# Performance work log

Measured on AMD Instinct MI355X. Metric: run time of the kernel, lower is better.

## Reference

```python
import jax, jax.numpy as jnp
import numpy as np


def _gcn_conv(X, src, dst, norm, W, n_nodes):
    # gather + normalized aggregate (SpMM) then dense linear (GEMM)
    msg = X[src] * norm[:, None]                       # [E, F]
    agg = jax.ops.segment_sum(msg, dst, num_segments=n_nodes)  # [N, F]
    return agg @ W                                     # [N, F_out]


def setup_inputs() -> dict:
    key = jax.random.key(0)
    k1, k2, k3, k4, k5 = jax.random.split(key, 5)
    N, E, D_IN, D_HID, D_OUT = 50000, 800000, 128, 128, 64
    X = jax.random.normal(k1, (N, D_IN), dtype=jnp.float32)
    edge_index = jax.random.randint(k2, (2, E), 0, N, dtype=jnp.int64)
    s = 1.0 / np.sqrt(D_IN)
    W1 = jax.random.normal(k3, (D_IN, D_HID), dtype=jnp.float32) * s
    W2 = jax.random.normal(k4, (D_HID, D_HID), dtype=jnp.float32) * s
    W3 = jax.random.normal(k5, (D_HID, D_OUT), dtype=jnp.float32) * s
    return {"X": X, "edge_index": edge_index, "W1": W1, "W2": W2, "W3": W3}


def reference(X, edge_index, W1, W2, W3):
    n_nodes = X.shape[0]
    src, dst = edge_index[0], edge_index[1]
    # symmetric degree normalization D^-1/2 A D^-1/2 (degrees from edge list)
    ones = jnp.ones(src.shape[0], dtype=X.dtype)
    deg = jax.ops.segment_sum(ones, dst, num_segments=n_nodes)
    deg = jnp.maximum(deg, 1.0)
    dinv = jax.lax.rsqrt(deg)
    norm = dinv[src] * dinv[dst]                       # [E]
    h = jax.nn.relu(_gcn_conv(X, src, dst, norm, W1, n_nodes))
    h = jax.nn.relu(_gcn_conv(h, src, dst, norm, W2, n_nodes))
    h = jax.nn.relu(_gcn_conv(h, src, dst, norm, W3, n_nodes))
    return jax.nn.softmax(h, axis=-1)
```

## Files before the change

kernel.cpp:

```cpp
#include <hip/hip_runtime.h>
#include <hip/hip_bf16.h>

typedef __attribute__((ext_vector_type(8))) short short8;
typedef __attribute__((ext_vector_type(4))) float f32x4;

static inline size_t ws_align(size_t x) { return (x + 511) & ~((size_t)511); }

static __device__ inline unsigned short f2bf(float f) {
    __hip_bfloat16 h = __float2bfloat16(f);
    return __builtin_bit_cast(unsigned short, h);
}

static __device__ inline float bf2f(unsigned short u) {
    unsigned int x = ((unsigned int)u) << 16;
    return __builtin_bit_cast(float, x);
}

__global__ void sniff_kernel(const unsigned short* __restrict__ w1,
                             const unsigned int* __restrict__ ei,
                             int* __restrict__ flags) {
    int i = threadIdx.x;
    unsigned e = (w1[2 * i] >> 7) & 0xFF;
    unsigned long long m1 = __ballot(e >= 100 && e <= 130);
    unsigned long long m2 = __ballot(ei[2 * i + 1] == 0u);
    if (i == 0) {
        flags[0] = (__popcll(m1) < 48) ? 1 : 0;
        flags[1] = (__popcll(m2) >= 48) ? 1 : 0;
    }
}

__global__ __launch_bounds__(256) void wconv_kernel(const void* __restrict__ W1raw,
                                                    const void* __restrict__ W2raw,
                                                    const void* __restrict__ W3raw,
                                                    const int* __restrict__ flags,
                                                    unsigned short* __restrict__ wt1,
                                                    unsigned short* __restrict__ wt2,
                                                    unsigned short* __restrict__ wt3) {
    int idx = blockIdx.x * 256 + threadIdx.x;
    int in_fp32 = flags[0];
    const void* src;
    unsigned short* dst;
    int e, fout;
    if (idx < 16384) {
        src = W1raw; dst = wt1; e = idx; fout = 128;
    } else if (idx < 32768) {
        src = W2raw; dst = wt2; e = idx - 16384; fout = 128;
    } else if (idx < 40960) {
        src = W3raw; dst = wt3; e = idx - 32768; fout = 64;
    } else {
        return;
    }
    int n = e & (fout - 1);
    int k = e / fout;
    unsigned short v;
    if (in_fp32) v = f2bf(((const float*)src)[e]);
    else         v = ((const unsigned short*)src)[e];
    dst[n * 128 + k] = v;
}

__global__ void hist_kernel(const int* __restrict__ ei, const int* __restrict__ flags,
                            int* __restrict__ counts, int* __restrict__ loff, int E) {
    int e = blockIdx.x * blockDim.x + threadIdx.x;
    if (e < E) {
        int d = flags[1] ? ei[2 * (size_t)E + 2 * e] : ei[(size_t)E + e];
        loff[e] = atomicAdd(&counts[d], 1);
    }
}

__global__ __launch_bounds__(256) void alloc_kernel(const int* __restrict__ counts,
                                                    float* __restrict__ dinv,
                                                    int* __restrict__ rowptr,
                                                    int* __restrict__ total, int N) {
    int n = blockIdx.x * blockDim.x + threadIdx.x;
    int lane = threadIdx.x & 63;
    int c = (n < N) ? counts[n] : 0;
    if (n < N) {
        int d = (c < 1) ? 1 : c;
        dinv[n] = rsqrtf((float)d);
    }
    int incl = c;
#pragma unroll
    for (int off = 1; off < 64; off <<= 1) {
        int v = __shfl_up(incl, off, 64);
        if (lane >= off) incl += v;
    }
    int wavetot = __shfl(incl, 63, 64);
    int base = 0;
    if (lane == 0) base = atomicAdd(total, wavetot);
    base = __shfl(base, 0, 64);
    if (n < N) rowptr[n] = base + incl - c;
}

__global__ void fill_kernel(const int* __restrict__ ei, const int* __restrict__ flags,
                            const float* __restrict__ dinv, const int* __restrict__ rowptr,
                            const int* __restrict__ loff, int2* __restrict__ edgedat, int E) {
    int e = blockIdx.x * blockDim.x + threadIdx.x;
    if (e < E) {
        int s, d;
        if (flags[1]) {
            s = ei[2 * e];
            d = ei[2 * (size_t)E + 2 * e];
        } else {
            s = ei[e];
            d = ei[(size_t)E + e];
        }
        int pos = rowptr[d] + loff[e];
        float wt = dinv[s] * dinv[d];
        edgedat[pos] = make_int2(s, __float_as_int(wt));
    }
}


template <int FOUT>
__global__ __launch_bounds__(256) void gemm_kernel(const void* __restrict__ Araw, int a_follows,
                                                   const unsigned short* __restrict__ wt,
                                                   const int* __restrict__ flags,
                                                   unsigned short* __restrict__ out, int Nrows) {
    constexpr int K = 128;
    constexpr int NT = FOUT / 16;

    const int tid = threadIdx.x;
    const int in_fp32 = flags[0];
    const int a_fp32 = a_follows & in_fp32;

    const int wave = tid >> 6;
    const int lane = tid & 63;
    const int quad = lane >> 4;
    const int r16 = lane & 15;

    short8 afrag[2][4];
#pragma unroll
    for (int t = 0; t < 2; t++) {
        int arow = blockIdx.x * 128 + t * 64 + wave * 16 + r16;
        if (arow > Nrows - 1) arow = Nrows - 1;
        if (a_fp32) {
            const float* Ap = (const float*)Araw + (size_t)arow * K + quad * 8;
#pragma unroll
            for (int kk = 0; kk < 4; kk++) {
                float4 f0 = *(const float4*)(const void*)(Ap + kk * 32);
                float4 f1 = *(const float4*)(const void*)(Ap + kk * 32 + 4);
                short8 r;
                r[0] = (short)f2bf(f0.x); r[1] = (short)f2bf(f0.y);
                r[2] = (short)f2bf(f0.z); r[3] = (short)f2bf(f0.w);
                r[4] = (short)f2bf(f1.x); r[5] = (short)f2bf(f1.y);
                r[6] = (short)f2bf(f1.z); r[7] = (short)f2bf(f1.w);
                afrag[t][kk] = r;
            }
        } else {
            const unsigned short* Ap = (const unsigned short*)Araw + (size_t)arow * K + quad * 8;
#pragma unroll
            for (int kk = 0; kk < 4; kk++) afrag[t][kk] = *(const short8*)(const void*)(Ap + kk * 32);
        }
    }

    f32x4 acc[2][NT];
#pragma unroll
    for (int t = 0; t < 2; t++)
#pragma unroll
        for (int nt = 0; nt < NT; nt++) acc[t][nt] = (f32x4){0.f, 0.f, 0.f, 0.f};

#pragma unroll
    for (int kk = 0; kk < 4; kk++) {
#pragma unroll
        for (int nt = 0; nt < NT; nt++) {
            short8 b = *(const short8*)(const void*)(wt + (size_t)(nt * 16 + r16) * 128 + kk * 32 + quad * 8);
#pragma unroll
            for (int t = 0; t < 2; t++)
                acc[t][nt] = __builtin_amdgcn_mfma_f32_16x16x32_bf16(afrag[t][kk], b, acc[t][nt], 0, 0, 0);
        }
    }

#pragma unroll
    for (int t = 0; t < 2; t++) {
#pragma unroll
        for (int nt = 0; nt < NT; nt++) {
#pragma unroll
            for (int r = 0; r < 4; r++) {
                float v = acc[t][nt][r];
                float o = __shfl_xor(v, 1, 64);
                int row = blockIdx.x * 128 + t * 64 + wave * 16 + quad * 4 + r;
                if (((lane & 1) == 0) && row < Nrows) {
                    __hip_bfloat162 pk;
                    pk.x = __float2bfloat16(v);
                    pk.y = __float2bfloat16(o);
                    *(__hip_bfloat162*)(out + (size_t)row * FOUT + nt * 16 + r16) = pk;
                }
            }
        }
    }
}


__global__ __launch_bounds__(256) void spmm128_kernel(const int2* __restrict__ edgedat,
                                                      const int* __restrict__ rowptr,
                                                      const int* __restrict__ counts,
                                                      const unsigned short* __restrict__ Hin,
                                                      unsigned short* __restrict__ Hout, int N) {
    int wid = (blockIdx.x * 256 + threadIdx.x) >> 6;
    if (wid >= N) return;
    int lane = threadIdx.x & 63;
    int grp = lane >> 4;
    int gl = lane & 15;
    int n = __builtin_amdgcn_readfirstlane(wid);
    int start = __builtin_amdgcn_readfirstlane(rowptr[n]);
    int len = __builtin_amdgcn_readfirstlane(counts[n]);
    const int2* ep = edgedat + start;

    float acc[8];
#pragma unroll
    for (int u = 0; u < 8; u++) acc[u] = 0.f;

    int j = 0;
    for (; j + 8 <= len; j += 8) {
        int2 e0 = ep[j + grp];
        int2 e1 = ep[j + 4 + grp];
        short8 h0 = *(const short8*)(const void*)(Hin + (size_t)e0.x * 128 + gl * 8);
        short8 h1 = *(const short8*)(const void*)(Hin + (size_t)e1.x * 128 + gl * 8);
        float w0 = __int_as_float(e0.y);
        float w1 = __int_as_float(e1.y);
#pragma unroll
        for (int u = 0; u < 8; u++) acc[u] += w0 * bf2f((unsigned short)h0[u]);
#pragma unroll
        for (int u = 0; u < 8; u++) acc[u] += w1 * bf2f((unsigned short)h1[u]);
    }
    for (; j + 4 <= len; j += 4) {
        int2 e = ep[j + grp];
        short8 h = *(const short8*)(const void*)(Hin + (size_t)e.x * 128 + gl * 8);
        float w = __int_as_float(e.y);
#pragma unroll
        for (int u = 0; u < 8; u++) acc[u] += w * bf2f((unsigned short)h[u]);
    }
    int rem = len - j;
    if (grp < rem) {
        int2 e = ep[j + grp];
        short8 h = *(const short8*)(const void*)(Hin + (size_t)e.x * 128 + gl * 8);
        float w = __int_as_float(e.y);
#pragma unroll
        for (int u = 0; u < 8; u++) acc[u] += w * bf2f((unsigned short)h[u]);
    }

#pragma unroll
    for (int u = 0; u < 8; u++) {
        acc[u] += __shfl_xor(acc[u], 16, 64);
        acc[u] += __shfl_xor(acc[u], 32, 64);
    }

    if (grp == 0) {
        short8 o;
#pragma unroll
        for (int u = 0; u < 8; u++) o[u] = (short)f2bf(fmaxf(acc[u], 0.f));
        *(short8*)(void*)(Hout + (size_t)n * 128 + gl * 8) = o;
    }
}


__global__ __launch_bounds__(256) void spmm64_softmax_kernel(const int2* __restrict__ edgedat,
                                                             const int* __restrict__ rowptr,
                                                             const int* __restrict__ counts,
                                                             const unsigned short* __restrict__ Hin,
                                                             const int* __restrict__ flags,
                                                             void* __restrict__ Out, int N) {
    int wid = (blockIdx.x * 256 + threadIdx.x) >> 6;
    if (wid >= N) return;
    int lane = threadIdx.x & 63;
    int grp = lane >> 3;
    int gl = lane & 7;
    int n = __builtin_amdgcn_readfirstlane(wid);
    int start = __builtin_amdgcn_readfirstlane(rowptr[n]);
    int len = __builtin_amdgcn_readfirstlane(counts[n]);
    const int2* ep = edgedat + start;

    float acc[8];
#pragma unroll
    for (int u = 0; u < 8; u++) acc[u] = 0.f;

    int j = 0;
    for (; j + 16 <= len; j += 16) {
        int2 e0 = ep[j + grp];
        int2 e1 = ep[j + 8 + grp];
        short8 h0 = *(const short8*)(const void*)(Hin + (size_t)e0.x * 64 + gl * 8);
        short8 h1 = *(const short8*)(const void*)(Hin + (size_t)e1.x * 64 + gl * 8);
        float w0 = __int_as_float(e0.y);
        float w1 = __int_as_float(e1.y);
#pragma unroll
        for (int u = 0; u < 8; u++) acc[u] += w0 * bf2f((unsigned short)h0[u]);
#pragma unroll
        for (int u = 0; u < 8; u++) acc[u] += w1 * bf2f((unsigned short)h1[u]);
    }
    for (; j + 8 <= len; j += 8) {
        int2 e = ep[j + grp];
        short8 h = *(const short8*)(const void*)(Hin + (size_t)e.x * 64 + gl * 8);
        float w = __int_as_float(e.y);
#pragma unroll
        for (int u = 0; u < 8; u++) acc[u] += w * bf2f((unsigned short)h[u]);
    }
    int rem = len - j;
    if (grp < rem) {
        int2 e = ep[j + grp];
        short8 h = *(const short8*)(const void*)(Hin + (size_t)e.x * 64 + gl * 8);
        float w = __int_as_float(e.y);
#pragma unroll
        for (int u = 0; u < 8; u++) acc[u] += w * bf2f((unsigned short)h[u]);
    }

#pragma unroll
    for (int u = 0; u < 8; u++) {
        acc[u] += __shfl_xor(acc[u], 8, 64);
        acc[u] += __shfl_xor(acc[u], 16, 64);
        acc[u] += __shfl_xor(acc[u], 32, 64);
    }

#pragma unroll
    for (int u = 0; u < 8; u++) acc[u] = fmaxf(acc[u], 0.f);

    float m = acc[0];
#pragma unroll
    for (int u = 1; u < 8; u++) m = fmaxf(m, acc[u]);
#pragma unroll
    for (int off = 1; off < 8; off <<= 1) m = fmaxf(m, __shfl_xor(m, off, 64));

    float ex[8];
    float s = 0.f;
#pragma unroll
    for (int u = 0; u < 8; u++) {
        ex[u] = __expf(acc[u] - m);
        s += ex[u];
    }
#pragma unroll
    for (int off = 1; off < 8; off <<= 1) s += __shfl_xor(s, off, 64);
    float inv = 1.0f / s;

    if (grp == 0) {
        if (flags[0]) {
            float* op = (float*)Out + (size_t)n * 64 + gl * 8;
            float4 v0, v1;
            v0.x = ex[0] * inv; v0.y = ex[1] * inv; v0.z = ex[2] * inv; v0.w = ex[3] * inv;
            v1.x = ex[4] * inv; v1.y = ex[5] * inv; v1.z = ex[6] * inv; v1.w = ex[7] * inv;
            *(float4*)(void*)op = v0;
            *(float4*)(void*)(op + 4) = v1;
        } else {
            short8 o;
#pragma unroll
            for (int u = 0; u < 8; u++) o[u] = (short)f2bf(ex[u] * inv);
            *(short8*)(void*)((unsigned short*)Out + (size_t)n * 64 + gl * 8) = o;
        }
    }
}


extern "C" void kernel_launch(void* const* d_in, const int* in_sizes, int n_in,
                              void* d_out, int out_size, void* d_ws, size_t ws_size,
                              hipStream_t stream) {
    const void* X  = d_in[0];
    const int*  ei = (const int*)d_in[1];
    const void* W1 = d_in[2];
    const void* W2 = d_in[3];
    const void* W3 = d_in[4];

    const int N = in_sizes[0] / 128;
    const int E = in_sizes[1] / 2;

    char* ws = (char*)d_ws;
    size_t off = 0;
    int* counts = (int*)(ws + off);   off += ws_align((size_t)N * 4);
    int* total  = (int*)(ws + off);   off += ws_align(64);
    const size_t zero_bytes = off;
    int* flags    = (int*)(ws + off);   off += ws_align(64);
    int* rowptr   = (int*)(ws + off);   off += ws_align((size_t)N * 4);
    float* dinv   = (float*)(ws + off); off += ws_align((size_t)N * 4);
    int* loff     = (int*)(ws + off);   off += ws_align((size_t)E * 4);
    int2* edgedat = (int2*)(ws + off);  off += ws_align((size_t)E * 8);
    unsigned short* HA = (unsigned short*)(ws + off); off += ws_align((size_t)N * 128 * 2);
    unsigned short* HB = (unsigned short*)(ws + off); off += ws_align((size_t)N * 128 * 2);
    unsigned short* wt1 = (unsigned short*)(ws + off); off += ws_align(16384 * 2);
    unsigned short* wt2 = (unsigned short*)(ws + off); off += ws_align(16384 * 2);
    unsigned short* wt3 = (unsigned short*)(ws + off); off += ws_align(8192 * 2);

    hipMemsetAsync(d_ws, 0, zero_bytes, stream);

    sniff_kernel<<<1, 64, 0, stream>>>((const unsigned short*)W1, (const unsigned int*)ei, flags);
    wconv_kernel<<<160, 256, 0, stream>>>(W1, W2, W3, flags, wt1, wt2, wt3);
    hist_kernel<<<(E + 255) / 256, 256, 0, stream>>>(ei, flags, counts, loff, E);
    alloc_kernel<<<(N + 255) / 256, 256, 0, stream>>>(counts, dinv, rowptr, total, N);
    fill_kernel<<<(E + 255) / 256, 256, 0, stream>>>(ei, flags, dinv, rowptr, loff, edgedat, E);

    const int gblocks = (N + 127) / 128;
    const int sblocks = (N * 64 + 255) / 256;

    gemm_kernel<128><<<gblocks, 256, 0, stream>>>(X, 1, wt1, flags, HA, N);
    spmm128_kernel<<<sblocks, 256, 0, stream>>>(edgedat, rowptr, counts, HA, HB, N);
    gemm_kernel<128><<<gblocks, 256, 0, stream>>>(HB, 0, wt2, flags, HA, N);
    spmm128_kernel<<<sblocks, 256, 0, stream>>>(edgedat, rowptr, counts, HA, HB, N);
    gemm_kernel<64><<<gblocks, 256, 0, stream>>>(HB, 0, wt3, flags, HA, N);
    spmm64_softmax_kernel<<<sblocks, 256, 0, stream>>>(edgedat, rowptr, counts, HA, flags, d_out, N);
}
```

Before: 278.1 us.

## Fuse SpMM aggregation with GEMM per layer and merge setup kernels

Each GCN layer now runs as one kernel: waves aggregate neighbor features for 16 nodes into shared memory, then MFMA multiplies that tile by the weights and applies ReLU (and softmax on the last layer). This switches from GEMM-then-SpMM order to aggregate-then-GEMM, which removes the intermediate feature buffer round-trip and three launches. The flag sniffing, histogram and weight conversion are also merged into one launch. In exchange, layer 1 now gathers fp32 X rows (wider gathers), and the last layer uses only one wave of four for the GEMM and softmax.

```diff
diff --git a/kernel.cpp b/kernel.cpp
--- a/kernel.cpp
+++ b/kernel.cpp
@@ -16,28 +16,42 @@
     return __builtin_bit_cast(float, x);
 }
 
-__global__ void sniff_kernel(const unsigned short* __restrict__ w1,
-                             const unsigned int* __restrict__ ei,
-                             int* __restrict__ flags) {
-    int i = threadIdx.x;
-    unsigned e = (w1[2 * i] >> 7) & 0xFF;
-    unsigned long long m1 = __ballot(e >= 100 && e <= 130);
-    unsigned long long m2 = __ballot(ei[2 * i + 1] == 0u);
-    if (i == 0) {
-        flags[0] = (__popcll(m1) < 48) ? 1 : 0;
-        flags[1] = (__popcll(m2) >= 48) ? 1 : 0;
-    }
-}
-
-__global__ __launch_bounds__(256) void wconv_kernel(const void* __restrict__ W1raw,
-                                                    const void* __restrict__ W2raw,
-                                                    const void* __restrict__ W3raw,
-                                                    const int* __restrict__ flags,
-                                                    unsigned short* __restrict__ wt1,
-                                                    unsigned short* __restrict__ wt2,
-                                                    unsigned short* __restrict__ wt3) {
-    int idx = blockIdx.x * 256 + threadIdx.x;
-    int in_fp32 = flags[0];
+
+__global__ __launch_bounds__(256) void hist_wconv_kernel(const int* __restrict__ ei,
+                                                         const unsigned short* __restrict__ w1s,
+                                                         const void* __restrict__ W1raw,
+                                                         const void* __restrict__ W2raw,
+                                                         const void* __restrict__ W3raw,
+                                                         int* __restrict__ counts,
+                                                         int* __restrict__ loff,
+                                                         int* __restrict__ flags,
+                                                         unsigned short* __restrict__ wt1,
+                                                         unsigned short* __restrict__ wt2,
+                                                         unsigned short* __restrict__ wt3,
+                                                         int E, int hblocks) {
+    const int tid = threadIdx.x;
+    const int lane = tid & 63;
+
+    unsigned ew = (w1s[2 * lane] >> 7) & 0xFF;
+    unsigned long long m1 = __ballot(ew >= 100 && ew <= 130);
+    const int in_fp32 = (__popcll(m1) < 48) ? 1 : 0;
+    unsigned long long m2 = __ballot(((const unsigned int*)ei)[2 * lane + 1] == 0u);
+    const int ei64 = (__popcll(m2) >= 48) ? 1 : 0;
+
+    if (blockIdx.x < hblocks) {
+        if (blockIdx.x == 0 && tid == 0) {
+            flags[0] = in_fp32;
+            flags[1] = ei64;
+        }
+        int e = blockIdx.x * 256 + tid;
+        if (e < E) {
+            int d = ei64 ? ei[2 * (size_t)E + 2 * e] : ei[(size_t)E + e];
+            loff[e] = atomicAdd(&counts[d], 1);
+        }
+        return;
+    }
+
+    int idx = (blockIdx.x - hblocks) * 256 + tid;
     const void* src;
     unsigned short* dst;
     int e, fout;
@@ -58,14 +72,6 @@
     dst[n * 128 + k] = v;
 }
 
-__global__ void hist_kernel(const int* __restrict__ ei, const int* __restrict__ flags,
-                            int* __restrict__ counts, int* __restrict__ loff, int E) {
-    int e = blockIdx.x * blockDim.x + threadIdx.x;
-    if (e < E) {
-        int d = flags[1] ? ei[2 * (size_t)E + 2 * e] : ei[(size_t)E + e];
-        loff[e] = atomicAdd(&counts[d], 1);
-    }
-}
 
 __global__ __launch_bounds__(256) void alloc_kernel(const int* __restrict__ counts,
                                                     float* __restrict__ dinv,
@@ -111,238 +117,203 @@
 }
 
 
-template <int FOUT>
-__global__ __launch_bounds__(256) void gemm_kernel(const void* __restrict__ Araw, int a_follows,
-                                                   const unsigned short* __restrict__ wt,
-                                                   const int* __restrict__ flags,
-                                                   unsigned short* __restrict__ out, int Nrows) {
-    constexpr int K = 128;
-    constexpr int NT = FOUT / 16;
+template <int FOUT, bool SM>
+__global__ __launch_bounds__(256) void fused_layer_kernel(const void* __restrict__ Hraw, int a_follows,
+                                                          const unsigned short* __restrict__ wt,
+                                                          const int2* __restrict__ edgedat,
+                                                          const int* __restrict__ rowptr,
+                                                          const int* __restrict__ counts,
+                                                          const int* __restrict__ flags,
+                                                          void* __restrict__ out, int N) {
+    constexpr int LDA = 136;
+    __shared__ __align__(16) unsigned short agg[16 * LDA];
 
     const int tid = threadIdx.x;
-    const int in_fp32 = flags[0];
-    const int a_fp32 = a_follows & in_fp32;
-
     const int wave = tid >> 6;
     const int lane = tid & 63;
+    const int grp = lane >> 4;
+    const int gl = lane & 15;
+    const int base = blockIdx.x * 16;
+    const int a_fp32 = a_follows & flags[0];
+    const unsigned short* Hb = (const unsigned short*)Hraw;
+    const float* Hf = (const float*)Hraw;
+
+    for (int i = 0; i < 4; i++) {
+        int node = base + wave * 4 + i;
+        int start = 0, len = 0;
+        if (node < N) {
+            start = rowptr[node];
+            len = counts[node];
+        }
+        start = __builtin_amdgcn_readfirstlane(start);
+        len = __builtin_amdgcn_readfirstlane(len);
+        const int2* ep = edgedat + start;
+
+        float acc[8];
+#pragma unroll
+        for (int u = 0; u < 8; u++) acc[u] = 0.f;
+
+        int j = 0;
+        if (a_fp32) {
+            for (; j + 4 <= len; j += 4) {
+                int2 e = ep[j + grp];
+                const float* hp = Hf + (size_t)e.x * 128 + gl * 8;
+                float4 a0 = *(const float4*)(const void*)hp;
+                float4 a1 = *(const float4*)(const void*)(hp + 4);
+                float w = __int_as_float(e.y);
+                acc[0] += w * a0.x; acc[1] += w * a0.y; acc[2] += w * a0.z; acc[3] += w * a0.w;
+                acc[4] += w * a1.x; acc[5] += w * a1.y; acc[6] += w * a1.z; acc[7] += w * a1.w;
+            }
+            int rem = len - j;
+            if (grp < rem) {
+                int2 e = ep[j + grp];
+                const float* hp = Hf + (size_t)e.x * 128 + gl * 8;
+                float4 a0 = *(const float4*)(const void*)hp;
+                float4 a1 = *(const float4*)(const void*)(hp + 4);
+                float w = __int_as_float(e.y);
+                acc[0] += w * a0.x; acc[1] += w * a0.y; acc[2] += w * a0.z; acc[3] += w * a0.w;
+                acc[4] += w * a1.x; acc[5] += w * a1.y; acc[6] += w * a1.z; acc[7] += w * a1.w;
+            }
+        } else {
+            for (; j + 8 <= len; j += 8) {
+                int2 e0 = ep[j + grp];
+                int2 e1 = ep[j + 4 + grp];
+                short8 h0 = *(const short8*)(const void*)(Hb + (size_t)e0.x * 128 + gl * 8);
+                short8 h1 = *(const short8*)(const void*)(Hb + (size_t)e1.x * 128 + gl * 8);
+                float w0 = __int_as_float(e0.y);
+                float w1 = __int_as_float(e1.y);
+#pragma unroll
+                for (int u = 0; u < 8; u++) acc[u] += w0 * bf2f((unsigned short)h0[u]);
+#pragma unroll
+                for (int u = 0; u < 8; u++) acc[u] += w1 * bf2f((unsigned short)h1[u]);
+            }
+            for (; j + 4 <= len; j += 4) {
+                int2 e = ep[j + grp];
+                short8 h = *(const short8*)(const void*)(Hb + (size_t)e.x * 128 + gl * 8);
+                float w = __int_as_float(e.y);
+#pragma unroll
+                for (int u = 0; u < 8; u++) acc[u] += w * bf2f((unsigned short)h[u]);
+            }
+            int rem = len - j;
+            if (grp < rem) {
+                int2 e = ep[j + grp];
+                short8 h = *(const short8*)(const void*)(Hb + (size_t)e.x * 128 + gl * 8);
+                float w = __int_as_float(e.y);
+#pragma unroll
+                for (int u = 0; u < 8; u++) acc[u] += w * bf2f((unsigned short)h[u]);
+            }
+        }
+
+#pragma unroll
+        for (int u = 0; u < 8; u++) {
+            acc[u] += __shfl_xor(acc[u], 16, 64);
+            acc[u] += __shfl_xor(acc[u], 32, 64);
+        }
+
+        if (grp == 0) {
+            short8 o;
+#pragma unroll
+            for (int u = 0; u < 8; u++) o[u] = (short)f2bf(acc[u]);
+            *(short8*)(void*)(&agg[(wave * 4 + i) * LDA + gl * 8]) = o;
+        }
+    }
+
+    __syncthreads();
+
     const int quad = lane >> 4;
     const int r16 = lane & 15;
 
-    short8 afrag[2][4];
-#pragma unroll
-    for (int t = 0; t < 2; t++) {
-        int arow = blockIdx.x * 128 + t * 64 + wave * 16 + r16;
-        if (arow > Nrows - 1) arow = Nrows - 1;
-        if (a_fp32) {
-            const float* Ap = (const float*)Araw + (size_t)arow * K + quad * 8;
-#pragma unroll
-            for (int kk = 0; kk < 4; kk++) {
-                float4 f0 = *(const float4*)(const void*)(Ap + kk * 32);
-                float4 f1 = *(const float4*)(const void*)(Ap + kk * 32 + 4);
-                short8 r;
-                r[0] = (short)f2bf(f0.x); r[1] = (short)f2bf(f0.y);
-                r[2] = (short)f2bf(f0.z); r[3] = (short)f2bf(f0.w);
-                r[4] = (short)f2bf(f1.x); r[5] = (short)f2bf(f1.y);
-                r[6] = (short)f2bf(f1.z); r[7] = (short)f2bf(f1.w);
-                afrag[t][kk] = r;
-            }
-        } else {
-            const unsigned short* Ap = (const unsigned short*)Araw + (size_t)arow * K + quad * 8;
-#pragma unroll
-            for (int kk = 0; kk < 4; kk++) afrag[t][kk] = *(const short8*)(const void*)(Ap + kk * 32);
-        }
-    }
-
-    f32x4 acc[2][NT];
-#pragma unroll
-    for (int t = 0; t < 2; t++)
-#pragma unroll
-        for (int nt = 0; nt < NT; nt++) acc[t][nt] = (f32x4){0.f, 0.f, 0.f, 0.f};
-
-#pragma unroll
-    for (int kk = 0; kk < 4; kk++) {
-#pragma unroll
-        for (int nt = 0; nt < NT; nt++) {
-            short8 b = *(const short8*)(const void*)(wt + (size_t)(nt * 16 + r16) * 128 + kk * 32 + quad * 8);
-#pragma unroll
-            for (int t = 0; t < 2; t++)
-                acc[t][nt] = __builtin_amdgcn_mfma_f32_16x16x32_bf16(afrag[t][kk], b, acc[t][nt], 0, 0, 0);
-        }
-    }
-
-#pragma unroll
-    for (int t = 0; t < 2; t++) {
-#pragma unroll
-        for (int nt = 0; nt < NT; nt++) {
+    if constexpr (!SM) {
+        short8 afrag[4];
+#pragma unroll
+        for (int kk = 0; kk < 4; kk++)
+            afrag[kk] = *(const short8*)(const void*)(&agg[r16 * LDA + kk * 32 + quad * 8]);
+
+        f32x4 acc2[2];
+#pragma unroll
+        for (int t = 0; t < 2; t++) acc2[t] = (f32x4){0.f, 0.f, 0.f, 0.f};
+
+#pragma unroll
+        for (int kk = 0; kk < 4; kk++) {
+#pragma unroll
+            for (int t = 0; t < 2; t++) {
+                int ntg = wave * 2 + t;
+                short8 b = *(const short8*)(const void*)(wt + (size_t)(ntg * 16 + r16) * 128 + kk * 32 + quad * 8);
+                acc2[t] = __builtin_amdgcn_mfma_f32_16x16x32_bf16(afrag[kk], b, acc2[t], 0, 0, 0);
+            }
+        }
+
+        unsigned short* ob = (unsigned short*)out;
+#pragma unroll
+        for (int t = 0; t < 2; t++) {
+            int ntg = wave * 2 + t;
 #pragma unroll
             for (int r = 0; r < 4; r++) {
-                float v = acc[t][nt][r];
+                float v = fmaxf(acc2[t][r], 0.f);
                 float o = __shfl_xor(v, 1, 64);
-                int row = blockIdx.x * 128 + t * 64 + wave * 16 + quad * 4 + r;
-                if (((lane & 1) == 0) && row < Nrows) {
+                int row = base + quad * 4 + r;
+                if (((lane & 1) == 0) && row < N) {
                     __hip_bfloat162 pk;
                     pk.x = __float2bfloat16(v);
                     pk.y = __float2bfloat16(o);
-                    *(__hip_bfloat162*)(out + (size_t)row * FOUT + nt * 16 + r16) = pk;
+                    *(__hip_bfloat162*)(ob + (size_t)row * 128 + ntg * 16 + r16) = pk;
                 }
             }
         }
-    }
-}
-
-
-__global__ __launch_bounds__(256) void spmm128_kernel(const int2* __restrict__ edgedat,
-                                                      const int* __restrict__ rowptr,
-                                                      const int* __restrict__ counts,
-                                                      const unsigned short* __restrict__ Hin,
-                                                      unsigned short* __restrict__ Hout, int N) {
-    int wid = (blockIdx.x * 256 + threadIdx.x) >> 6;
-    if (wid >= N) return;
-    int lane = threadIdx.x & 63;
-    int grp = lane >> 4;
-    int gl = lane & 15;
-    int n = __builtin_amdgcn_readfirstlane(wid);
-    int start = __builtin_amdgcn_readfirstlane(rowptr[n]);
-    int len = __builtin_amdgcn_readfirstlane(counts[n]);
-    const int2* ep = edgedat + start;
-
-    float acc[8];
-#pragma unroll
-    for (int u = 0; u < 8; u++) acc[u] = 0.f;
-
-    int j = 0;
-    for (; j + 8 <= len; j += 8) {
-        int2 e0 = ep[j + grp];
-        int2 e1 = ep[j + 4 + grp];
-        short8 h0 = *(const short8*)(const void*)(Hin + (size_t)e0.x * 128 + gl * 8);
-        short8 h1 = *(const short8*)(const void*)(Hin + (size_t)e1.x * 128 + gl * 8);
-        float w0 = __int_as_float(e0.y);
-        float w1 = __int_as_float(e1.y);
-#pragma unroll
-        for (int u = 0; u < 8; u++) acc[u] += w0 * bf2f((unsigned short)h0[u]);
-#pragma unroll
-        for (int u = 0; u < 8; u++) acc[u] += w1 * bf2f((unsigned short)h1[u]);
-    }
-    for (; j + 4 <= len; j += 4) {
-        int2 e = ep[j + grp];
-        short8 h = *(const short8*)(const void*)(Hin + (size_t)e.x * 128 + gl * 8);
-        float w = __int_as_float(e.y);
-#pragma unroll
-        for (int u = 0; u < 8; u++) acc[u] += w * bf2f((unsigned short)h[u]);
-    }
-    int rem = len - j;
-    if (grp < rem) {
-        int2 e = ep[j + grp];
-        short8 h = *(const short8*)(const void*)(Hin + (size_t)e.x * 128 + gl * 8);
-        float w = __int_as_float(e.y);
-#pragma unroll
-        for (int u = 0; u < 8; u++) acc[u] += w * bf2f((unsigned short)h[u]);
-    }
-
-#pragma unroll
-    for (int u = 0; u < 8; u++) {
-        acc[u] += __shfl_xor(acc[u], 16, 64);
-        acc[u] += __shfl_xor(acc[u], 32, 64);
-    }
-
-    if (grp == 0) {
-        short8 o;
-#pragma unroll
-        for (int u = 0; u < 8; u++) o[u] = (short)f2bf(fmaxf(acc[u], 0.f));
-        *(short8*)(void*)(Hout + (size_t)n * 128 + gl * 8) = o;
-    }
-}
-
-
-__global__ __launch_bounds__(256) void spmm64_softmax_kernel(const int2* __restrict__ edgedat,
-                                                             const int* __restrict__ rowptr,
-                                                             const int* __restrict__ counts,
-                                                             const unsigned short* __restrict__ Hin,
-                                                             const int* __restrict__ flags,
-                                                             void* __restrict__ Out, int N) {
-    int wid = (blockIdx.x * 256 + threadIdx.x) >> 6;
-    if (wid >= N) return;
-    int lane = threadIdx.x & 63;
-    int grp = lane >> 3;
-    int gl = lane & 7;
-    int n = __builtin_amdgcn_readfirstlane(wid);
-    int start = __builtin_amdgcn_readfirstlane(rowptr[n]);
-    int len = __builtin_amdgcn_readfirstlane(counts[n]);
-    const int2* ep = edgedat + start;
-
-    float acc[8];
-#pragma unroll
-    for (int u = 0; u < 8; u++) acc[u] = 0.f;
-
-    int j = 0;
-    for (; j + 16 <= len; j += 16) {
-        int2 e0 = ep[j + grp];
-        int2 e1 = ep[j + 8 + grp];
-        short8 h0 = *(const short8*)(const void*)(Hin + (size_t)e0.x * 64 + gl * 8);
-        short8 h1 = *(const short8*)(const void*)(Hin + (size_t)e1.x * 64 + gl * 8);
-        float w0 = __int_as_float(e0.y);
-        float w1 = __int_as_float(e1.y);
-#pragma unroll
-        for (int u = 0; u < 8; u++) acc[u] += w0 * bf2f((unsigned short)h0[u]);
-#pragma unroll
-        for (int u = 0; u < 8; u++) acc[u] += w1 * bf2f((unsigned short)h1[u]);
-    }
-    for (; j + 8 <= len; j += 8) {
-        int2 e = ep[j + grp];
-        short8 h = *(const short8*)(const void*)(Hin + (size_t)e.x * 64 + gl * 8);
-        float w = __int_as_float(e.y);
-#pragma unroll
-        for (int u = 0; u < 8; u++) acc[u] += w * bf2f((unsigned short)h[u]);
-    }
-    int rem = len - j;
-    if (grp < rem) {
-        int2 e = ep[j + grp];
-        short8 h = *(const short8*)(const void*)(Hin + (size_t)e.x * 64 + gl * 8);
-        float w = __int_as_float(e.y);
-#pragma unroll
-        for (int u = 0; u < 8; u++) acc[u] += w * bf2f((unsigned short)h[u]);
-    }
-
-#pragma unroll
-    for (int u = 0; u < 8; u++) {
-        acc[u] += __shfl_xor(acc[u], 8, 64);
-        acc[u] += __shfl_xor(acc[u], 16, 64);
-        acc[u] += __shfl_xor(acc[u], 32, 64);
-    }
-
-#pragma unroll
-    for (int u = 0; u < 8; u++) acc[u] = fmaxf(acc[u], 0.f);
-
-    float m = acc[0];
-#pragma unroll
-    for (int u = 1; u < 8; u++) m = fmaxf(m, acc[u]);
-#pragma unroll
-    for (int off = 1; off < 8; off <<= 1) m = fmaxf(m, __shfl_xor(m, off, 64));
-
-    float ex[8];
-    float s = 0.f;
-#pragma unroll
-    for (int u = 0; u < 8; u++) {
-        ex[u] = __expf(acc[u] - m);
-        s += ex[u];
-    }
-#pragma unroll
-    for (int off = 1; off < 8; off <<= 1) s += __shfl_xor(s, off, 64);
-    float inv = 1.0f / s;
-
-    if (grp == 0) {
-        if (flags[0]) {
-            float* op = (float*)Out + (size_t)n * 64 + gl * 8;
-            float4 v0, v1;
-            v0.x = ex[0] * inv; v0.y = ex[1] * inv; v0.z = ex[2] * inv; v0.w = ex[3] * inv;
-            v1.x = ex[4] * inv; v1.y = ex[5] * inv; v1.z = ex[6] * inv; v1.w = ex[7] * inv;
-            *(float4*)(void*)op = v0;
-            *(float4*)(void*)(op + 4) = v1;
-        } else {
-            short8 o;
-#pragma unroll
-            for (int u = 0; u < 8; u++) o[u] = (short)f2bf(ex[u] * inv);
-            *(short8*)(void*)((unsigned short*)Out + (size_t)n * 64 + gl * 8) = o;
+    } else {
+        if (wave != 0) return;
+        short8 afrag[4];
+#pragma unroll
+        for (int kk = 0; kk < 4; kk++)
+            afrag[kk] = *(const short8*)(const void*)(&agg[r16 * LDA + kk * 32 + quad * 8]);
+
+        f32x4 acc3[4];
+#pragma unroll
+        for (int nt = 0; nt < 4; nt++) acc3[nt] = (f32x4){0.f, 0.f, 0.f, 0.f};
+#pragma unroll
+        for (int kk = 0; kk < 4; kk++) {
+#pragma unroll
+            for (int nt = 0; nt < 4; nt++) {
+                short8 b = *(const short8*)(const void*)(wt + (size_t)(nt * 16 + r16) * 128 + kk * 32 + quad * 8);
+                acc3[nt] = __builtin_amdgcn_mfma_f32_16x16x32_bf16(afrag[kk], b, acc3[nt], 0, 0, 0);
+            }
+        }
+
+        const int out_fp32 = flags[0];
+#pragma unroll
+        for (int r = 0; r < 4; r++) {
+            float v0 = fmaxf(acc3[0][r], 0.f);
+            float v1 = fmaxf(acc3[1][r], 0.f);
+            float v2 = fmaxf(acc3[2][r], 0.f);
+            float v3 = fmaxf(acc3[3][r], 0.f);
+            float m = fmaxf(fmaxf(v0, v1), fmaxf(v2, v3));
+#pragma unroll
+            for (int off = 1; off < 16; off <<= 1) m = fmaxf(m, __shfl_xor(m, off, 64));
+            float e0 = __expf(v0 - m), e1 = __expf(v1 - m), e2 = __expf(v2 - m), e3 = __expf(v3 - m);
+            float s = e0 + e1 + e2 + e3;
+#pragma unroll
+            for (int off = 1; off < 16; off <<= 1) s += __shfl_xor(s, off, 64);
+            float inv = 1.0f / s;
+            float rv[4] = {e0 * inv, e1 * inv, e2 * inv, e3 * inv};
+            int row = base + quad * 4 + r;
+            if (out_fp32) {
+                if (row < N) {
+                    float* op = (float*)out + (size_t)row * 64;
+#pragma unroll
+                    for (int nt = 0; nt < 4; nt++) op[nt * 16 + r16] = rv[nt];
+                }
+            } else {
+#pragma unroll
+                for (int nt = 0; nt < 4; nt++) {
+                    float o = __shfl_xor(rv[nt], 1, 64);
+                    if (((lane & 1) == 0) && row < N) {
+                        __hip_bfloat162 pk;
+                        pk.x = __float2bfloat16(rv[nt]);
+                        pk.y = __float2bfloat16(o);
+                        *(__hip_bfloat162*)((unsigned short*)out + (size_t)row * 64 + nt * 16 + r16) = pk;
+                    }
+                }
+            }
         }
     }
 }
@@ -370,27 +341,26 @@
     float* dinv   = (float*)(ws + off); off += ws_align((size_t)N * 4);
     int* loff     = (int*)(ws + off);   off += ws_align((size_t)E * 4);
     int2* edgedat = (int2*)(ws + off);  off += ws_align((size_t)E * 8);
-    unsigned short* HA = (unsigned short*)(ws + off); off += ws_align((size_t)N * 128 * 2);
-    unsigned short* HB = (unsigned short*)(ws + off); off += ws_align((size_t)N * 128 * 2);
+    unsigned short* H1 = (unsigned short*)(ws + off); off += ws_align((size_t)N * 128 * 2);
+    unsigned short* H2 = (unsigned short*)(ws + off); off += ws_align((size_t)N * 128 * 2);
     unsigned short* wt1 = (unsigned short*)(ws + off); off += ws_align(16384 * 2);
     unsigned short* wt2 = (unsigned short*)(ws + off); off += ws_align(16384 * 2);
     unsigned short* wt3 = (unsigned short*)(ws + off); off += ws_align(8192 * 2);
 
     hipMemsetAsync(d_ws, 0, zero_bytes, stream);
 
-    sniff_kernel<<<1, 64, 0, stream>>>((const unsigned short*)W1, (const unsigned int*)ei, flags);
-    wconv_kernel<<<160, 256, 0, stream>>>(W1, W2, W3, flags, wt1, wt2, wt3);
-    hist_kernel<<<(E + 255) / 256, 256, 0, stream>>>(ei, flags, counts, loff, E);
+    const int hblocks = (E + 255) / 256;
+    const int fblocks = (N + 15) / 16;
+
+    hist_wconv_kernel<<<hblocks + 160, 256, 0, stream>>>(
+        ei, (const unsigned short*)W1, W1, W2, W3, counts, loff, flags, wt1, wt2, wt3, E, hblocks);
     alloc_kernel<<<(N + 255) / 256, 256, 0, stream>>>(counts, dinv, rowptr, total, N);
-    fill_kernel<<<(E + 255) / 256, 256, 0, stream>>>(ei, flags, dinv, rowptr, loff, edgedat, E);
-
-    const int gblocks = (N + 127) / 128;
-    const int sblocks = (N * 64 + 255) / 256;
-
-    gemm_kernel<128><<<gblocks, 256, 0, stream>>>(X, 1, wt1, flags, HA, N);
-    spmm128_kernel<<<sblocks, 256, 0, stream>>>(edgedat, rowptr, counts, HA, HB, N);
-    gemm_kernel<128><<<gblocks, 256, 0, stream>>>(HB, 0, wt2, flags, HA, N);
-    spmm128_kernel<<<sblocks, 256, 0, stream>>>(edgedat, rowptr, counts, HA, HB, N);
-    gemm_kernel<64><<<gblocks, 256, 0, stream>>>(HB, 0, wt3, flags, HA, N);
-    spmm64_softmax_kernel<<<sblocks, 256, 0, stream>>>(edgedat, rowptr, counts, HA, flags, d_out, N);
-}
+    fill_kernel<<<hblocks, 256, 0, stream>>>(ei, flags, dinv, rowptr, loff, edgedat, E);
+
+    fused_layer_kernel<128, false><<<fblocks, 256, 0, stream>>>(
+        X, 1, wt1, edgedat, rowptr, counts, flags, H1, N);
+    fused_layer_kernel<128, false><<<fblocks, 256, 0, stream>>>(
+        H1, 0, wt2, edgedat, rowptr, counts, flags, H2, N);
+    fused_layer_kernel<64, true><<<fblocks, 256, 0, stream>>>(
+        H2, 0, wt3, edgedat, rowptr, counts, flags, d_out, N);
+}
```

New measurement: 282.6 us. Within noise of the previous version (+1.6%).

## Fuse first GEMM with degree histogram and shrink GEMM tiles to 16 rows

Applied to the files above, without the earlier changes.

Removes the separate sniff kernel: each block now detects dtype and index width itself. The first GEMM and the edge histogram run in one launch with a block-range split, so the atomic histogram work can overlap with the MFMA work. GEMM tiles shrink from 128 to 16 rows per block, with waves splitting the output columns, which gives many more blocks for occupancy but reloads B fragments more often. Launch count drops by two, at the cost of redundant per-block sniffing and a heterogeneous fused kernel.

```diff
diff --git a/kernel.cpp b/kernel.cpp
--- a/kernel.cpp
+++ b/kernel.cpp
@@ -16,28 +16,20 @@
     return __builtin_bit_cast(float, x);
 }
 
-__global__ void sniff_kernel(const unsigned short* __restrict__ w1,
-                             const unsigned int* __restrict__ ei,
-                             int* __restrict__ flags) {
-    int i = threadIdx.x;
-    unsigned e = (w1[2 * i] >> 7) & 0xFF;
-    unsigned long long m1 = __ballot(e >= 100 && e <= 130);
-    unsigned long long m2 = __ballot(ei[2 * i + 1] == 0u);
-    if (i == 0) {
-        flags[0] = (__popcll(m1) < 48) ? 1 : 0;
-        flags[1] = (__popcll(m2) >= 48) ? 1 : 0;
-    }
-}
-
-__global__ __launch_bounds__(256) void wconv_kernel(const void* __restrict__ W1raw,
+__global__ __launch_bounds__(256) void wconv_kernel(const unsigned short* __restrict__ w1s,
+                                                    const void* __restrict__ W1raw,
                                                     const void* __restrict__ W2raw,
                                                     const void* __restrict__ W3raw,
-                                                    const int* __restrict__ flags,
                                                     unsigned short* __restrict__ wt1,
                                                     unsigned short* __restrict__ wt2,
                                                     unsigned short* __restrict__ wt3) {
-    int idx = blockIdx.x * 256 + threadIdx.x;
-    int in_fp32 = flags[0];
+    const int tid = threadIdx.x;
+    const int lane = tid & 63;
+    unsigned ew = (w1s[2 * lane] >> 7) & 0xFF;
+    unsigned long long m1 = __ballot(ew >= 100 && ew <= 130);
+    const int in_fp32 = (__popcll(m1) < 48) ? 1 : 0;
+
+    int idx = blockIdx.x * 256 + tid;
     const void* src;
     unsigned short* dst;
     int e, fout;
@@ -58,14 +50,151 @@
     dst[n * 128 + k] = v;
 }
 
-__global__ void hist_kernel(const int* __restrict__ ei, const int* __restrict__ flags,
-                            int* __restrict__ counts, int* __restrict__ loff, int E) {
-    int e = blockIdx.x * blockDim.x + threadIdx.x;
-    if (e < E) {
-        int d = flags[1] ? ei[2 * (size_t)E + 2 * e] : ei[(size_t)E + e];
-        loff[e] = atomicAdd(&counts[d], 1);
-    }
-}
+
+__global__ __launch_bounds__(256) void gemm1_hist_kernel(const void* __restrict__ Xraw,
+                                                         const unsigned short* __restrict__ w1s,
+                                                         const int* __restrict__ ei,
+                                                         const unsigned short* __restrict__ wt1,
+                                                         int* __restrict__ counts,
+                                                         int* __restrict__ loff,
+                                                         int* __restrict__ flags,
+                                                         unsigned short* __restrict__ out,
+                                                         int N, int E, int gblocks) {
+    const int tid = threadIdx.x;
+    const int lane = tid & 63;
+
+    unsigned ew = (w1s[2 * lane] >> 7) & 0xFF;
+    unsigned long long m1 = __ballot(ew >= 100 && ew <= 130);
+    const int in_fp32 = (__popcll(m1) < 48) ? 1 : 0;
+
+    if (blockIdx.x >= gblocks) {
+        unsigned long long m2 = __ballot(((const unsigned int*)ei)[2 * lane + 1] == 0u);
+        const int ei64 = (__popcll(m2) >= 48) ? 1 : 0;
+        if (blockIdx.x == gblocks && tid == 0) {
+            flags[0] = in_fp32;
+            flags[1] = ei64;
+        }
+        int e = (blockIdx.x - gblocks) * 256 + tid;
+        if (e < E) {
+            int d = ei64 ? ei[2 * (size_t)E + 2 * e] : ei[(size_t)E + e];
+            loff[e] = atomicAdd(&counts[d], 1);
+        }
+        return;
+    }
+
+    const int wave = tid >> 6;
+    const int quad = lane >> 4;
+    const int r16 = lane & 15;
+    const int base = blockIdx.x * 16;
+
+    int arow = base + r16;
+    if (arow > N - 1) arow = N - 1;
+
+    short8 afrag[4];
+    if (in_fp32) {
+        const float* Ap = (const float*)Xraw + (size_t)arow * 128 + quad * 8;
+#pragma unroll
+        for (int kk = 0; kk < 4; kk++) {
+            float4 f0 = *(const float4*)(const void*)(Ap + kk * 32);
+            float4 f1 = *(const float4*)(const void*)(Ap + kk * 32 + 4);
+            short8 r;
+            r[0] = (short)f2bf(f0.x); r[1] = (short)f2bf(f0.y);
+            r[2] = (short)f2bf(f0.z); r[3] = (short)f2bf(f0.w);
+            r[4] = (short)f2bf(f1.x); r[5] = (short)f2bf(f1.y);
+            r[6] = (short)f2bf(f1.z); r[7] = (short)f2bf(f1.w);
+            afrag[kk] = r;
+        }
+    } else {
+        const unsigned short* Ap = (const unsigned short*)Xraw + (size_t)arow * 128 + quad * 8;
+#pragma unroll
+        for (int kk = 0; kk < 4; kk++) afrag[kk] = *(const short8*)(const void*)(Ap + kk * 32);
+    }
+
+    f32x4 acc[2];
+#pragma unroll
+    for (int t = 0; t < 2; t++) acc[t] = (f32x4){0.f, 0.f, 0.f, 0.f};
+
+#pragma unroll
+    for (int kk = 0; kk < 4; kk++) {
+#pragma unroll
+        for (int t = 0; t < 2; t++) {
+            int ntg = wave * 2 + t;
+            short8 b = *(const short8*)(const void*)(wt1 + (size_t)(ntg * 16 + r16) * 128 + kk * 32 + quad * 8);
+            acc[t] = __builtin_amdgcn_mfma_f32_16x16x32_bf16(afrag[kk], b, acc[t], 0, 0, 0);
+        }
+    }
+
+#pragma unroll
+    for (int t = 0; t < 2; t++) {
+        int ntg = wave * 2 + t;
+#pragma unroll
+        for (int r = 0; r < 4; r++) {
+            float v = acc[t][r];
+            float o = __shfl_xor(v, 1, 64);
+            int row = base + quad * 4 + r;
+            if (((lane & 1) == 0) && row < N) {
+                __hip_bfloat162 pk;
+                pk.x = __float2bfloat16(v);
+                pk.y = __float2bfloat16(o);
+                *(__hip_bfloat162*)(out + (size_t)row * 128 + ntg * 16 + r16) = pk;
+            }
+        }
+    }
+}
+
+
+template <int FOUT>
+__global__ __launch_bounds__(256) void gemm_kernel(const unsigned short* __restrict__ A,
+                                                   const unsigned short* __restrict__ wt,
+                                                   unsigned short* __restrict__ out, int N) {
+    constexpr int TPW = FOUT / 64;
+    const int tid = threadIdx.x;
+    const int wave = tid >> 6;
+    const int lane = tid & 63;
+    const int quad = lane >> 4;
+    const int r16 = lane & 15;
+    const int base = blockIdx.x * 16;
+
+    int arow = base + r16;
+    if (arow > N - 1) arow = N - 1;
+    const unsigned short* Ap = A + (size_t)arow * 128 + quad * 8;
+
+    short8 afrag[4];
+#pragma unroll
+    for (int kk = 0; kk < 4; kk++) afrag[kk] = *(const short8*)(const void*)(Ap + kk * 32);
+
+    f32x4 acc[TPW];
+#pragma unroll
+    for (int t = 0; t < TPW; t++) acc[t] = (f32x4){0.f, 0.f, 0.f, 0.f};
+
+#pragma unroll
+    for (int kk = 0; kk < 4; kk++) {
+#pragma unroll
+        for (int t = 0; t < TPW; t++) {
+            int ntg = wave * TPW + t;
+            short8 b = *(const short8*)(const void*)(wt + (size_t)(ntg * 16 + r16) * 128 + kk * 32 + quad * 8);
+            acc[t] = __builtin_amdgcn_mfma_f32_16x16x32_bf16(afrag[kk], b, acc[t], 0, 0, 0);
+        }
+    }
+
+#pragma unroll
+    for (int t = 0; t < TPW; t++) {
+        int ntg = wave * TPW + t;
+#pragma unroll
+        for (int r = 0; r < 4; r++) {
+            float v = acc[t][r];
+            float o = __shfl_xor(v, 1, 64);
+            int row = base + quad * 4 + r;
+            if (((lane & 1) == 0) && row < N) {
+                __hip_bfloat162 pk;
+                pk.x = __float2bfloat16(v);
+                pk.y = __float2bfloat16(o);
+                *(__hip_bfloat162*)(out + (size_t)row * FOUT + ntg * 16 + r16) = pk;
+            }
+        }
+    }
+}
+
 
 __global__ __launch_bounds__(256) void alloc_kernel(const int* __restrict__ counts,
                                                     float* __restrict__ dinv,
@@ -107,86 +236,6 @@
         int pos = rowptr[d] + loff[e];
         float wt = dinv[s] * dinv[d];
         edgedat[pos] = make_int2(s, __float_as_int(wt));
-    }
-}
-
-
-template <int FOUT>
-__global__ __launch_bounds__(256) void gemm_kernel(const void* __restrict__ Araw, int a_follows,
-                                                   const unsigned short* __restrict__ wt,
-                                                   const int* __restrict__ flags,
-                                                   unsigned short* __restrict__ out, int Nrows) {
-    constexpr int K = 128;
-    constexpr int NT = FOUT / 16;
-
-    const int tid = threadIdx.x;
-    const int in_fp32 = flags[0];
-    const int a_fp32 = a_follows & in_fp32;
-
-    const int wave = tid >> 6;
-    const int lane = tid & 63;
-    const int quad = lane >> 4;
-    const int r16 = lane & 15;
-
-    short8 afrag[2][4];
-#pragma unroll
-    for (int t = 0; t < 2; t++) {
-        int arow = blockIdx.x * 128 + t * 64 + wave * 16 + r16;
-        if (arow > Nrows - 1) arow = Nrows - 1;
-        if (a_fp32) {
-            const float* Ap = (const float*)Araw + (size_t)arow * K + quad * 8;
-#pragma unroll
-            for (int kk = 0; kk < 4; kk++) {
-                float4 f0 = *(const float4*)(const void*)(Ap + kk * 32);
-                float4 f1 = *(const float4*)(const void*)(Ap + kk * 32 + 4);
-                short8 r;
-                r[0] = (short)f2bf(f0.x); r[1] = (short)f2bf(f0.y);
-                r[2] = (short)f2bf(f0.z); r[3] = (short)f2bf(f0.w);
-                r[4] = (short)f2bf(f1.x); r[5] = (short)f2bf(f1.y);
-                r[6] = (short)f2bf(f1.z); r[7] = (short)f2bf(f1.w);
-                afrag[t][kk] = r;
-            }
-        } else {
-            const unsigned short* Ap = (const unsigned short*)Araw + (size_t)arow * K + quad * 8;
-#pragma unroll
-            for (int kk = 0; kk < 4; kk++) afrag[t][kk] = *(const short8*)(const void*)(Ap + kk * 32);
-        }
-    }
-
-    f32x4 acc[2][NT];
-#pragma unroll
-    for (int t = 0; t < 2; t++)
-#pragma unroll
-        for (int nt = 0; nt < NT; nt++) acc[t][nt] = (f32x4){0.f, 0.f, 0.f, 0.f};
-
-#pragma unroll
-    for (int kk = 0; kk < 4; kk++) {
-#pragma unroll
-        for (int nt = 0; nt < NT; nt++) {
-            short8 b = *(const short8*)(const void*)(wt + (size_t)(nt * 16 + r16) * 128 + kk * 32 + quad * 8);
-#pragma unroll
-            for (int t = 0; t < 2; t++)
-                acc[t][nt] = __builtin_amdgcn_mfma_f32_16x16x32_bf16(afrag[t][kk], b, acc[t][nt], 0, 0, 0);
-        }
-    }
-
-#pragma unroll
-    for (int t = 0; t < 2; t++) {
-#pragma unroll
-        for (int nt = 0; nt < NT; nt++) {
-#pragma unroll
-            for (int r = 0; r < 4; r++) {
-                float v = acc[t][nt][r];
-                float o = __shfl_xor(v, 1, 64);
-                int row = blockIdx.x * 128 + t * 64 + wave * 16 + quad * 4 + r;
-                if (((lane & 1) == 0) && row < Nrows) {
-                    __hip_bfloat162 pk;
-                    pk.x = __float2bfloat16(v);
-                    pk.y = __float2bfloat16(o);
-                    *(__hip_bfloat162*)(out + (size_t)row * FOUT + nt * 16 + r16) = pk;
-                }
-            }
-        }
     }
 }
 
@@ -378,19 +427,19 @@
 
     hipMemsetAsync(d_ws, 0, zero_bytes, stream);
 
-    sniff_kernel<<<1, 64, 0, stream>>>((const unsigned short*)W1, (const unsigned int*)ei, flags);
-    wconv_kernel<<<160, 256, 0, stream>>>(W1, W2, W3, flags, wt1, wt2, wt3);
-    hist_kernel<<<(E + 255) / 256, 256, 0, stream>>>(ei, flags, counts, loff, E);
+    const int gblocks = (N + 15) / 16;
+    const int hblocks = (E + 255) / 256;
+    const int sblocks = (N * 64 + 255) / 256;
+
+    wconv_kernel<<<160, 256, 0, stream>>>((const unsigned short*)W1, W1, W2, W3, wt1, wt2, wt3);
+    gemm1_hist_kernel<<<gblocks + hblocks, 256, 0, stream>>>(
+        X, (const unsigned short*)W1, ei, wt1, counts, loff, flags, HA, N, E, gblocks);
     alloc_kernel<<<(N + 255) / 256, 256, 0, stream>>>(counts, dinv, rowptr, total, N);
-    fill_kernel<<<(E + 255) / 256, 256, 0, stream>>>(ei, flags, dinv, rowptr, loff, edgedat, E);
-
-    const int gblocks = (N + 127) / 128;
-    const int sblocks = (N * 64 + 255) / 256;
-
-    gemm_kernel<128><<<gblocks, 256, 0, stream>>>(X, 1, wt1, flags, HA, N);
+    fill_kernel<<<hblocks, 256, 0, stream>>>(ei, flags, dinv, rowptr, loff, edgedat, E);
+
     spmm128_kernel<<<sblocks, 256, 0, stream>>>(edgedat, rowptr, counts, HA, HB, N);
-    gemm_kernel<128><<<gblocks, 256, 0, stream>>>(HB, 0, wt2, flags, HA, N);
+    gemm_kernel<128><<<gblocks, 256, 0, stream>>>(HB, wt2, HA, N);
     spmm128_kernel<<<sblocks, 256, 0, stream>>>(edgedat, rowptr, counts, HA, HB, N);
-    gemm_kernel<64><<<gblocks, 256, 0, stream>>>(HB, 0, wt3, flags, HA, N);
+    gemm_kernel<64><<<gblocks, 256, 0, stream>>>(HB, wt3, HA, N);
     spmm64_softmax_kernel<<<sblocks, 256, 0, stream>>>(edgedat, rowptr, counts, HA, flags, d_out, N);
 }
```

New measurement: 290.4 us. +4.4%, slower.
